# Performance work log

Measured on AMD Instinct MI355X. Metric: run time of the kernel, lower is better.

## Reference

```python
import jax, jax.numpy as jnp
import numpy as np

N_HEAD = 8
HEAD_DIM = 128
WINDOW = 512
ROPE_BASE = 10000.0


def _rope_tables(T, dtype):
    # inv_freq: [head_dim/2]
    inv_freq = 1.0 / (ROPE_BASE ** (jnp.arange(0, HEAD_DIM, 2, dtype=jnp.float32) / HEAD_DIM))
    t = jnp.arange(T, dtype=jnp.float32)
    freqs = jnp.einsum('i,j->ij', t, inv_freq)          # [T, head_dim/2]
    emb = jnp.concatenate([freqs, freqs], axis=-1)       # [T, head_dim]
    return jnp.cos(emb).astype(dtype), jnp.sin(emb).astype(dtype)


def _rotate_half(x):
    d = x.shape[-1] // 2
    return jnp.concatenate([-x[..., d:], x[..., :d]], axis=-1)


def setup_inputs() -> dict:
    key = jax.random.key(0)
    k1, k2, k3 = jax.random.split(key, 3)
    B, T, C = 2, 4096, 1024
    x = jax.random.normal(k1, (B, T, C), dtype=jnp.float32)
    w_qkv = jax.random.normal(k2, (3 * C, C), dtype=jnp.float32) * (1.0 / np.sqrt(C))
    w_o = jax.random.normal(k3, (C, C), dtype=jnp.float32) * (1.0 / np.sqrt(C))
    return {"x": x, "w_qkv": w_qkv, "w_o": w_o}


def reference(x, w_qkv, w_o):
    B, T, C = x.shape
    scale = 1.0 / np.sqrt(HEAD_DIM)
    qkv = x @ w_qkv.T                                     # [B,T,3C]
    q, k, v = jnp.split(qkv, 3, axis=-1)
    # [B, H, T, D]
    q = q.reshape(B, T, N_HEAD, HEAD_DIM).transpose(0, 2, 1, 3)
    k = k.reshape(B, T, N_HEAD, HEAD_DIM).transpose(0, 2, 1, 3)
    v = v.reshape(B, T, N_HEAD, HEAD_DIM).transpose(0, 2, 1, 3)
    cos, sin = _rope_tables(T, x.dtype)                   # [T, D]
    cos = cos[None, None]
    sin = sin[None, None]
    q = q * cos + _rotate_half(q) * sin
    k = k * cos + _rotate_half(k) * sin
    attn = jnp.einsum('bhqd,bhkd->bhqk', q, k) * scale    # [B,H,T,T]
    i = jnp.arange(T)[:, None]
    j = jnp.arange(T)[None, :]
    # causal (j<=i) AND sliding window triu(diag=-W) (j >= i - W)
    keep = (j <= i) & (j >= i - WINDOW)
    neg = jnp.finfo(attn.dtype).min
    attn = jnp.where(keep[None, None], attn, neg)
    attn = jax.nn.softmax(attn, axis=-1)
    out = jnp.einsum('bhqk,bhkd->bhqd', attn, v)          # [B,H,T,D]
    out = out.transpose(0, 2, 1, 3).reshape(B, T, C)
    return out @ w_o.T
```

## Files before the change

kernel.cpp:

```cpp
#include <hip/hip_runtime.h>
#include <hip/hip_bf16.h>

typedef unsigned short us;
typedef __attribute__((ext_vector_type(8))) __bf16 bf16x8;
typedef __attribute__((ext_vector_type(4))) float f32x4;

#define MFMA16(a, b, c) __builtin_amdgcn_mfma_f32_16x16x32_bf16(a, b, c, 0, 0, 0)

static __device__ __forceinline__ us f2bf(float f) {
  __hip_bfloat16 h = __float2bfloat16(f);
  return __builtin_bit_cast(us, h);
}

static __device__ __forceinline__ void gll16(const us* g, us* l) {
  __builtin_amdgcn_global_load_lds((const __attribute__((address_space(1))) void*)g,
                                   (__attribute__((address_space(3))) void*)l,
                                   16, 0, 0);
}

__global__ void cast_kernel(const float* __restrict__ in, us* __restrict__ out, int n4) {
  int i = blockIdx.x * blockDim.x + threadIdx.x;
  if (i >= n4) return;
  float4 v = ((const float4*)in)[i];
  ushort4 o;
  o.x = f2bf(v.x); o.y = f2bf(v.y); o.z = f2bf(v.z); o.w = f2bf(v.w);
  ((ushort4*)out)[i] = o;
}

__global__ void rope_table_kernel(float* __restrict__ ct, float* __restrict__ st) {
  int t = blockIdx.x, d = threadIdx.x;
  float ang = (float)t * exp2f((float)d * -0.20762050593046014f);
  float s, c;
  sincosf(ang, &s, &c);
  ct[t * 64 + d] = c;
  st[t * 64 + d] = s;
}

__global__ __launch_bounds__(256, 2)
void qkv_rope_kernel(const us* __restrict__ A, const us* __restrict__ B,
                     const float* __restrict__ ctab, const float* __restrict__ stab,
                     us* __restrict__ qb, us* __restrict__ kb, us* __restrict__ vtb) {
  __shared__ __align__(16) char smem_raw[128 * 132 * 4];
  us* sA = (us*)smem_raw;
  us* sB = sA + 128 * 64;
  float* sC = (float*)smem_raw;

  const int tid = threadIdx.x;
  const int lane = tid & 63;
  const int wave = tid >> 6;
  const int l15 = lane & 15;
  const int lq = lane >> 4;
  const int m0 = blockIdx.x * 128;
  const int n0 = blockIdx.y * 128;
  const int wm = (wave & 1) * 64;
  const int wn2 = (wave >> 1) * 32;

  f32x4 acc[4][4] = {};

  for (int k0 = 0; k0 < 1024; k0 += 64) {
    for (int i = 0; i < 4; ++i) {
      int c = wave * 4 + i;
      int P = c * 64 + lane;
      int row = P >> 3;
      int cb = (P & 7) ^ (row & 7);
      gll16(A + (size_t)(m0 + row) * 1024 + k0 + cb * 8, sA + c * 512);
      gll16(B + (size_t)(n0 + row) * 1024 + k0 + cb * 8, sB + c * 512);
    }
    __syncthreads();
#pragma unroll
    for (int kk = 0; kk < 64; kk += 32) {
      const int cbr = (kk + lq * 8) >> 3;
      bf16x8 av[4], bv[4];
#pragma unroll
      for (int mt = 0; mt < 4; ++mt) {
        int m = wm + mt * 16 + l15;
        av[mt] = *(const bf16x8*)(sA + (m * 8 + (cbr ^ (m & 7))) * 8);
      }
#pragma unroll
      for (int nt = 0; nt < 4; ++nt) {
        int n = wn2 + (nt & 1) * 16 + (nt >> 1) * 64 + l15;
        bv[nt] = *(const bf16x8*)(sB + (n * 8 + (cbr ^ (n & 7))) * 8);
      }
#pragma unroll
      for (int mt = 0; mt < 4; ++mt)
#pragma unroll
        for (int nt = 0; nt < 4; ++nt)
          acc[mt][nt] = MFMA16(av[mt], bv[nt], acc[mt][nt]);
    }
    __syncthreads();
  }

  const int b = m0 >> 12;
  const int t0 = m0 & 4095;
  const int which = blockIdx.y >> 3;
  const int h = blockIdx.y & 7;

  if (which < 2) {
    us* outp = (which == 0) ? qb : kb;
    const size_t obase = ((size_t)(b * 8 + h)) * 4096 * 128;
#pragma unroll
    for (int mt = 0; mt < 4; ++mt)
#pragma unroll
      for (int r = 0; r < 4; ++r) {
        const int row = wm + mt * 16 + lq * 4 + r;
        const int tg = t0 + row;
        const float* cp = ctab + tg * 64 + wn2 + l15;
        const float* sp = stab + tg * 64 + wn2 + l15;
        const float c0 = cp[0], c1 = cp[16], s0 = sp[0], s1 = sp[16];
        us* orow = outp + obase + (size_t)tg * 128 + wn2 + l15;
#pragma unroll
        for (int nt = 0; nt < 4; ++nt) {
          float x = acc[mt][nt][r];
          float xp = acc[mt][nt ^ 2][r];
          float rot = (nt < 2) ? -xp : xp;
          float y = x * ((nt & 1) ? c1 : c0) + rot * ((nt & 1) ? s1 : s0);
          orow[(nt & 1) * 16 + (nt >> 1) * 64] = f2bf(y);
        }
      }
  } else {
#pragma unroll
    for (int mt = 0; mt < 4; ++mt)
#pragma unroll
      for (int nt = 0; nt < 4; ++nt) {
        const int col = wn2 + (nt & 1) * 16 + (nt >> 1) * 64 + l15;
#pragma unroll
        for (int r = 0; r < 4; ++r)
          sC[(wm + mt * 16 + lq * 4 + r) * 129 + col] = acc[mt][nt][r];
      }
    __syncthreads();
    for (int r = 0; r < 8; ++r) {
      int d = (tid >> 4) + r * 16;
      int tl0 = (tid & 15) * 8;
      union { us u[8]; uint4 v; } tmp;
#pragma unroll
      for (int j = 0; j < 8; ++j)
        tmp.u[j] = f2bf(sC[(tl0 + j) * 129 + d]);
      *(uint4*)(vtb + ((size_t)((b * 8 + h) * 128 + d)) * 4096 + t0 + tl0) = tmp.v;
    }
  }
}

template <int MASK>
__device__ __forceinline__ void p_write(f32x4 (&s)[4], us* __restrict__ sP,
                                        int t0, int tj0, int wm16, int lq, int l15) {
  const float C2 = 0.08838834764831845f * 1.4426950408889634f;
#pragma unroll
  for (int nt = 0; nt < 4; ++nt) {
    const int jg = tj0 + nt * 16 + l15;
#pragma unroll
    for (int r = 0; r < 4; ++r) {
      const int rowl = wm16 + lq * 4 + r;
      float v = s[nt][r];
      if (MASK == 1) v = (jg + 512 >= t0 + rowl) ? v : -3.0e38f;
      if (MASK == 2) v = (jg <= t0 + rowl) ? v : -3.0e38f;
      sP[rowl * 72 + nt * 16 + l15] = f2bf(exp2f(v * C2));
    }
  }
}

__global__ __launch_bounds__(256, 2)
void flash_kernel(const us* __restrict__ qg, const us* __restrict__ kg,
                  const us* __restrict__ vg, us* __restrict__ ao) {
  __shared__ us sK[2 * 64 * 128];
  __shared__ us sV[2 * 128 * 64];
  __shared__ us sP[64 * 72];

  const int tid = threadIdx.x;
  const int lane = tid & 63;
  const int wave = tid >> 6;
  const int l15 = lane & 15;
  const int lq = lane >> 4;
  const int qx = blockIdx.x;
  const int h = blockIdx.y;
  const int b = blockIdx.z;
  const int t0 = qx * 64;
  const size_t bh = (size_t)(b * 8 + h);
  const int wm16 = wave * 16;

  bf16x8 qf[4];
#pragma unroll
  for (int ks = 0; ks < 4; ++ks)
    qf[ks] = *(const bf16x8*)(qg + (bh * 4096 + t0 + wm16 + l15) * 128 + ks * 32 + lq * 8);

  union { us u[8]; bf16x8 v; } one_u;
#pragma unroll
  for (int i = 0; i < 8; ++i) one_u.u[i] = 0x3F80;
  const bf16x8 vone = one_u.v;

  f32x4 o[9] = {};

  const int lo = t0 - 512;
  const int jtmin = (lo <= 0) ? 0 : (lo >> 6);
  const int jtmax = t0 >> 6;
  const bool wmask = (t0 >= 512);

  auto stage = [&](int jt, int buf) {
    const int tj0 = jt * 64;
    us* dK = sK + buf * 8192;
    us* dV = sV + buf * 8192;
    for (int i = 0; i < 4; ++i) {
      int c = wave * 4 + i;
      int P = c * 64 + lane;
      int rowK = P >> 4;
      int cbK = (P & 15) ^ (rowK & 15);
      gll16(kg + (bh * 4096 + tj0 + rowK) * 128 + cbK * 8, dK + c * 512);
      int rowV = P >> 3;
      int cbV = (P & 7) ^ (rowV & 7);
      gll16(vg + (bh * 128 + rowV) * 4096 + tj0 + cbV * 8, dV + c * 512);
    }
  };

  stage(jtmin, 0);
  int cur = 0;

  for (int jt = jtmin; jt <= jtmax; ++jt) {
    __syncthreads();
    if (jt < jtmax) stage(jt + 1, cur ^ 1);

    const int tj0 = jt * 64;
    const us* sKc = sK + cur * 8192;
    const us* sVc = sV + cur * 8192;

    f32x4 s[4] = {};
#pragma unroll
    for (int ks = 0; ks < 4; ++ks) {
      const int cbr = ks * 4 + lq;
#pragma unroll
      for (int nt = 0; nt < 4; ++nt) {
        int n = nt * 16 + l15;
        bf16x8 bk = *(const bf16x8*)(sKc + (n * 16 + (cbr ^ (n & 15))) * 8);
        s[nt] = MFMA16(qf[ks], bk, s[nt]);
      }
    }

    if (jt == jtmax)               p_write<2>(s, sP, t0, tj0, wm16, lq, l15);
    else if (wmask && jt == jtmin) p_write<1>(s, sP, t0, tj0, wm16, lq, l15);
    else                           p_write<0>(s, sP, t0, tj0, wm16, lq, l15);

#pragma unroll
    for (int ks = 0; ks < 2; ++ks) {
      const int ko = ks * 32 + lq * 8;
      const int slot = ks * 4 + lq;
      bf16x8 ap = *(const bf16x8*)(sP + (wm16 + l15) * 72 + ko);
#pragma unroll
      for (int dt = 0; dt < 8; ++dt) {
        int dd = dt * 16 + l15;
        bf16x8 bv = *(const bf16x8*)(sVc + (dd * 8 + (slot ^ (dd & 7))) * 8);
        o[dt] = MFMA16(ap, bv, o[dt]);
      }
      o[8] = MFMA16(ap, vone, o[8]);
    }
    cur ^= 1;
  }

#pragma unroll
  for (int r = 0; r < 4; ++r) {
    const float inv = 1.0f / o[8][r];
    const int rowl = wm16 + lq * 4 + r;
    const size_t base = ((size_t)b * 4096 + t0 + rowl) * 1024 + h * 128;
#pragma unroll
    for (int dt = 0; dt < 8; ++dt)
      ao[base + dt * 16 + l15] = f2bf(o[dt][r] * inv);
  }
}

__global__ __launch_bounds__(256, 2)
void out_proj_kernel(const us* __restrict__ A, const us* __restrict__ B, float* __restrict__ C) {
  __shared__ us sA[128 * 64];
  __shared__ us sB[128 * 64];
  const int tid = threadIdx.x;
  const int lane = tid & 63;
  const int wave = tid >> 6;
  const int l15 = lane & 15;
  const int lq = lane >> 4;
  const int m0 = blockIdx.x * 128;
  const int n0 = blockIdx.y * 128;
  const int wm = (wave & 1) * 64;
  const int wn = (wave >> 1) * 64;
  f32x4 acc[4][4] = {};
  for (int k0 = 0; k0 < 1024; k0 += 64) {
    for (int i = 0; i < 4; ++i) {
      int c = wave * 4 + i;
      int P = c * 64 + lane;
      int row = P >> 3;
      int cb = (P & 7) ^ (row & 7);
      gll16(A + (size_t)(m0 + row) * 1024 + k0 + cb * 8, sA + c * 512);
      gll16(B + (size_t)(n0 + row) * 1024 + k0 + cb * 8, sB + c * 512);
    }
    __syncthreads();
#pragma unroll
    for (int kk = 0; kk < 64; kk += 32) {
      const int cbr = (kk + lq * 8) >> 3;
      bf16x8 av[4], bv[4];
#pragma unroll
      for (int mt = 0; mt < 4; ++mt) {
        int m = wm + mt * 16 + l15;
        av[mt] = *(const bf16x8*)(sA + (m * 8 + (cbr ^ (m & 7))) * 8);
      }
#pragma unroll
      for (int nt = 0; nt < 4; ++nt) {
        int n = wn + nt * 16 + l15;
        bv[nt] = *(const bf16x8*)(sB + (n * 8 + (cbr ^ (n & 7))) * 8);
      }
#pragma unroll
      for (int mt = 0; mt < 4; ++mt)
#pragma unroll
        for (int nt = 0; nt < 4; ++nt)
          acc[mt][nt] = MFMA16(av[mt], bv[nt], acc[mt][nt]);
    }
    __syncthreads();
  }
#pragma unroll
  for (int mt = 0; mt < 4; ++mt)
#pragma unroll
    for (int nt = 0; nt < 4; ++nt)
#pragma unroll
      for (int r = 0; r < 4; ++r)
        C[(size_t)(m0 + wm + mt * 16 + lq * 4 + r) * 1024 + (n0 + wn + nt * 16 + l15)] =
            acc[mt][nt][r];
}

extern "C" void kernel_launch(void* const* d_in, const int* in_sizes, int n_in,
                              void* d_out, int out_size, void* d_ws, size_t ws_size,
                              hipStream_t stream) {
  const float* x     = (const float*)d_in[0];
  const float* w_qkv = (const float*)d_in[1];
  const float* w_o   = (const float*)d_in[2];
  float* out = (float*)d_out;

  us* xb  = (us*)d_ws;
  us* wqb = xb  + (size_t)8192 * 1024;
  us* wob = wqb + (size_t)3072 * 1024;
  us* qb  = wob + (size_t)1024 * 1024;
  us* kb  = qb  + (size_t)2 * 8 * 4096 * 128;
  us* vtb = kb  + (size_t)2 * 8 * 4096 * 128;
  us* aob = vtb + (size_t)2 * 8 * 4096 * 128;
  float* ctab = (float*)(aob + (size_t)8192 * 1024);
  float* stab = ctab + (size_t)4096 * 64;

  rope_table_kernel<<<4096, 64, 0, stream>>>(ctab, stab);
  cast_kernel<<<8192, 256, 0, stream>>>(x, xb, 8192 * 1024 / 4);
  cast_kernel<<<3072, 256, 0, stream>>>(w_qkv, wqb, 3072 * 1024 / 4);
  cast_kernel<<<1024, 256, 0, stream>>>(w_o, wob, 1024 * 1024 / 4);
  qkv_rope_kernel<<<dim3(64, 24), 256, 0, stream>>>(xb, wqb, ctab, stab, qb, kb, vtb);
  flash_kernel<<<dim3(64, 8, 2), 256, 0, stream>>>(qb, kb, vtb, aob);
  out_proj_kernel<<<dim3(64, 8), 256, 0, stream>>>(aob, wob, out);
}
```

Before: 232.7 us.

## Enlarge flash query tile to 128 rows, fuse prep kernels, stage Q/K stores

```diff
diff --git a/kernel.cpp b/kernel.cpp
--- a/kernel.cpp
+++ b/kernel.cpp
@@ -18,22 +18,32 @@
                                    16, 0, 0);
 }
 
-__global__ void cast_kernel(const float* __restrict__ in, us* __restrict__ out, int n4) {
-  int i = blockIdx.x * blockDim.x + threadIdx.x;
-  if (i >= n4) return;
-  float4 v = ((const float4*)in)[i];
-  ushort4 o;
-  o.x = f2bf(v.x); o.y = f2bf(v.y); o.z = f2bf(v.z); o.w = f2bf(v.w);
-  ((ushort4*)out)[i] = o;
-}
-
-__global__ void rope_table_kernel(float* __restrict__ ct, float* __restrict__ st) {
-  int t = blockIdx.x, d = threadIdx.x;
-  float ang = (float)t * exp2f((float)d * -0.20762050593046014f);
-  float s, c;
-  sincosf(ang, &s, &c);
-  ct[t * 64 + d] = c;
-  st[t * 64 + d] = s;
+__global__ void prep_kernel(const float* __restrict__ x, const float* __restrict__ wq,
+                            const float* __restrict__ wo, us* __restrict__ xb,
+                            us* __restrict__ wqb, us* __restrict__ wob,
+                            float* __restrict__ ct, float* __restrict__ st) {
+  const int blk = blockIdx.x;
+  const int tid = threadIdx.x;
+  if (blk < 12288) {
+    const float* in;
+    us* out;
+    int i;
+    if (blk < 8192)      { in = x;  out = xb;  i = blk * 256 + tid; }
+    else if (blk < 11264){ in = wq; out = wqb; i = (blk - 8192) * 256 + tid; }
+    else                 { in = wo; out = wob; i = (blk - 11264) * 256 + tid; }
+    float4 v = ((const float4*)in)[i];
+    ushort4 o;
+    o.x = f2bf(v.x); o.y = f2bf(v.y); o.z = f2bf(v.z); o.w = f2bf(v.w);
+    ((ushort4*)out)[i] = o;
+  } else {
+    int i = (blk - 12288) * 256 + tid;
+    int t = i >> 6, d = i & 63;
+    float ang = (float)t * exp2f((float)d * -0.20762050593046014f);
+    float s, c;
+    sincosf(ang, &s, &c);
+    ct[i] = c;
+    st[i] = s;
+  }
 }
 
 __global__ __launch_bounds__(256, 2)
@@ -44,6 +54,7 @@
   us* sA = (us*)smem_raw;
   us* sB = sA + 128 * 64;
   float* sC = (float*)smem_raw;
+  us* sCus = (us*)smem_raw;
 
   const int tid = threadIdx.x;
   const int lane = tid & 63;
@@ -107,16 +118,22 @@
         const float* cp = ctab + tg * 64 + wn2 + l15;
         const float* sp = stab + tg * 64 + wn2 + l15;
         const float c0 = cp[0], c1 = cp[16], s0 = sp[0], s1 = sp[16];
-        us* orow = outp + obase + (size_t)tg * 128 + wn2 + l15;
 #pragma unroll
         for (int nt = 0; nt < 4; ++nt) {
-          float x = acc[mt][nt][r];
+          float xv = acc[mt][nt][r];
           float xp = acc[mt][nt ^ 2][r];
           float rot = (nt < 2) ? -xp : xp;
-          float y = x * ((nt & 1) ? c1 : c0) + rot * ((nt & 1) ? s1 : s0);
-          orow[(nt & 1) * 16 + (nt >> 1) * 64] = f2bf(y);
+          float y = xv * ((nt & 1) ? c1 : c0) + rot * ((nt & 1) ? s1 : s0);
+          sCus[row * 136 + wn2 + (nt & 1) * 16 + (nt >> 1) * 64 + l15] = f2bf(y);
         }
       }
+    __syncthreads();
+    for (int r = 0; r < 8; ++r) {
+      int row = (tid >> 4) + r * 16;
+      int col = (tid & 15) * 8;
+      uint4 v = *(const uint4*)(sCus + row * 136 + col);
+      *(uint4*)(outp + obase + (size_t)(t0 + row) * 128 + col) = v;
+    }
   } else {
 #pragma unroll
     for (int mt = 0; mt < 4; ++mt)
@@ -141,29 +158,34 @@
 }
 
 template <int MASK>
-__device__ __forceinline__ void p_write(f32x4 (&s)[4], us* __restrict__ sP,
-                                        int t0, int tj0, int wm16, int lq, int l15) {
+__device__ __forceinline__ void p_write(f32x4 (&s)[2][4], us* __restrict__ sP,
+                                        int t0, int tj0, int wm2, int lq, int l15) {
   const float C2 = 0.08838834764831845f * 1.4426950408889634f;
 #pragma unroll
-  for (int nt = 0; nt < 4; ++nt) {
-    const int jg = tj0 + nt * 16 + l15;
-#pragma unroll
-    for (int r = 0; r < 4; ++r) {
-      const int rowl = wm16 + lq * 4 + r;
-      float v = s[nt][r];
-      if (MASK == 1) v = (jg + 512 >= t0 + rowl) ? v : -3.0e38f;
-      if (MASK == 2) v = (jg <= t0 + rowl) ? v : -3.0e38f;
-      sP[rowl * 72 + nt * 16 + l15] = f2bf(exp2f(v * C2));
-    }
-  }
+  for (int mt = 0; mt < 2; ++mt)
+#pragma unroll
+    for (int nt = 0; nt < 4; ++nt) {
+      const int jg = tj0 + nt * 16 + l15;
+      const int cb = (nt * 16 + l15) >> 3;
+      const int co = l15 & 7;
+#pragma unroll
+      for (int r = 0; r < 4; ++r) {
+        const int rowl = wm2 + mt * 16 + lq * 4 + r;
+        float v = s[mt][nt][r];
+        if (MASK == 1) v = (jg + 512 >= t0 + rowl) ? v : -3.0e38f;
+        if (MASK == 2) v = (jg <= t0 + rowl) ? v : -3.0e38f;
+        sP[rowl * 64 + ((cb ^ (rowl & 7)) * 8) + co] = f2bf(exp2f(v * C2));
+      }
+    }
 }
 
 __global__ __launch_bounds__(256, 2)
 void flash_kernel(const us* __restrict__ qg, const us* __restrict__ kg,
                   const us* __restrict__ vg, us* __restrict__ ao) {
-  __shared__ us sK[2 * 64 * 128];
-  __shared__ us sV[2 * 128 * 64];
-  __shared__ us sP[64 * 72];
+  __shared__ us smem[40960];
+  us* sK = smem;
+  us* sV = smem + 16384;
+  us* sP = smem + 32768;
 
   const int tid = threadIdx.x;
   const int lane = tid & 63;
@@ -173,25 +195,28 @@
   const int qx = blockIdx.x;
   const int h = blockIdx.y;
   const int b = blockIdx.z;
-  const int t0 = qx * 64;
+  const int t0 = qx * 128;
   const size_t bh = (size_t)(b * 8 + h);
-  const int wm16 = wave * 16;
-
-  bf16x8 qf[4];
-#pragma unroll
-  for (int ks = 0; ks < 4; ++ks)
-    qf[ks] = *(const bf16x8*)(qg + (bh * 4096 + t0 + wm16 + l15) * 128 + ks * 32 + lq * 8);
+  const int wm2 = wave * 32;
+
+  bf16x8 qf[2][4];
+#pragma unroll
+  for (int mt = 0; mt < 2; ++mt)
+#pragma unroll
+    for (int ks = 0; ks < 4; ++ks)
+      qf[mt][ks] = *(const bf16x8*)(qg + (bh * 4096 + t0 + wm2 + mt * 16 + l15) * 128 +
+                                    ks * 32 + lq * 8);
 
   union { us u[8]; bf16x8 v; } one_u;
 #pragma unroll
   for (int i = 0; i < 8; ++i) one_u.u[i] = 0x3F80;
   const bf16x8 vone = one_u.v;
 
-  f32x4 o[9] = {};
+  f32x4 o[2][9] = {};
 
   const int lo = t0 - 512;
   const int jtmin = (lo <= 0) ? 0 : (lo >> 6);
-  const int jtmax = t0 >> 6;
+  const int jtmax = (t0 + 127) >> 6;
   const bool wmask = (t0 >= 512);
 
   auto stage = [&](int jt, int buf) {
@@ -221,7 +246,7 @@
     const us* sKc = sK + cur * 8192;
     const us* sVc = sV + cur * 8192;
 
-    f32x4 s[4] = {};
+    f32x4 s[2][4] = {};
 #pragma unroll
     for (int ks = 0; ks < 4; ++ks) {
       const int cbr = ks * 4 + lq;
@@ -229,39 +254,45 @@
       for (int nt = 0; nt < 4; ++nt) {
         int n = nt * 16 + l15;
         bf16x8 bk = *(const bf16x8*)(sKc + (n * 16 + (cbr ^ (n & 15))) * 8);
-        s[nt] = MFMA16(qf[ks], bk, s[nt]);
-      }
-    }
-
-    if (jt == jtmax)               p_write<2>(s, sP, t0, tj0, wm16, lq, l15);
-    else if (wmask && jt == jtmin) p_write<1>(s, sP, t0, tj0, wm16, lq, l15);
-    else                           p_write<0>(s, sP, t0, tj0, wm16, lq, l15);
+#pragma unroll
+        for (int mt = 0; mt < 2; ++mt)
+          s[mt][nt] = MFMA16(qf[mt][ks], bk, s[mt][nt]);
+      }
+    }
+
+    if (jt >= jtmax - 1)               p_write<2>(s, sP, t0, tj0, wm2, lq, l15);
+    else if (wmask && jt <= jtmin + 1) p_write<1>(s, sP, t0, tj0, wm2, lq, l15);
+    else                               p_write<0>(s, sP, t0, tj0, wm2, lq, l15);
 
 #pragma unroll
     for (int ks = 0; ks < 2; ++ks) {
-      const int ko = ks * 32 + lq * 8;
-      const int slot = ks * 4 + lq;
-      bf16x8 ap = *(const bf16x8*)(sP + (wm16 + l15) * 72 + ko);
-#pragma unroll
-      for (int dt = 0; dt < 8; ++dt) {
-        int dd = dt * 16 + l15;
-        bf16x8 bv = *(const bf16x8*)(sVc + (dd * 8 + (slot ^ (dd & 7))) * 8);
-        o[dt] = MFMA16(ap, bv, o[dt]);
-      }
-      o[8] = MFMA16(ap, vone, o[8]);
+#pragma unroll
+      for (int mt = 0; mt < 2; ++mt) {
+        bf16x8 ap = *(const bf16x8*)(sP + (wm2 + mt * 16 + l15) * 64 +
+                                     (((ks * 4 + lq) ^ (l15 & 7)) * 8));
+#pragma unroll
+        for (int dt = 0; dt < 8; ++dt) {
+          int dd = dt * 16 + l15;
+          bf16x8 bv = *(const bf16x8*)(sVc + (dd * 8 + ((ks * 4 + lq) ^ (dd & 7))) * 8);
+          o[mt][dt] = MFMA16(ap, bv, o[mt][dt]);
+        }
+        o[mt][8] = MFMA16(ap, vone, o[mt][8]);
+      }
     }
     cur ^= 1;
   }
 
 #pragma unroll
-  for (int r = 0; r < 4; ++r) {
-    const float inv = 1.0f / o[8][r];
-    const int rowl = wm16 + lq * 4 + r;
-    const size_t base = ((size_t)b * 4096 + t0 + rowl) * 1024 + h * 128;
-#pragma unroll
-    for (int dt = 0; dt < 8; ++dt)
-      ao[base + dt * 16 + l15] = f2bf(o[dt][r] * inv);
-  }
+  for (int mt = 0; mt < 2; ++mt)
+#pragma unroll
+    for (int r = 0; r < 4; ++r) {
+      const float inv = 1.0f / o[mt][8][r];
+      const int rowl = wm2 + mt * 16 + lq * 4 + r;
+      const size_t base = ((size_t)b * 4096 + t0 + rowl) * 1024 + h * 128;
+#pragma unroll
+      for (int dt = 0; dt < 8; ++dt)
+        ao[base + dt * 16 + l15] = f2bf(o[mt][dt][r] * inv);
+    }
 }
 
 __global__ __launch_bounds__(256, 2)
@@ -338,11 +369,8 @@
   float* ctab = (float*)(aob + (size_t)8192 * 1024);
   float* stab = ctab + (size_t)4096 * 64;
 
-  rope_table_kernel<<<4096, 64, 0, stream>>>(ctab, stab);
-  cast_kernel<<<8192, 256, 0, stream>>>(x, xb, 8192 * 1024 / 4);
-  cast_kernel<<<3072, 256, 0, stream>>>(w_qkv, wqb, 3072 * 1024 / 4);
-  cast_kernel<<<1024, 256, 0, stream>>>(w_o, wob, 1024 * 1024 / 4);
+  prep_kernel<<<13312, 256, 0, stream>>>(x, w_qkv, w_o, xb, wqb, wob, ctab, stab);
   qkv_rope_kernel<<<dim3(64, 24), 256, 0, stream>>>(xb, wqb, ctab, stab, qb, kb, vtb);
-  flash_kernel<<<dim3(64, 8, 2), 256, 0, stream>>>(qb, kb, vtb, aob);
+  flash_kernel<<<dim3(32, 8, 2), 256, 0, stream>>>(qb, kb, vtb, aob);
   out_proj_kernel<<<dim3(64, 8), 256, 0, stream>>>(aob, wob, out);
 }
```

Measured after the change: 210.7 us. 9.4% less time.
